# Kernel tuning notes

Hardware: AMD Instinct MI355X
Metric: run time of the kernel (lower is better)

The kernel has to match this reference:

```python
import jax, jax.numpy as jnp
import numpy as np


def _gcn_conv(x, W, b, src, dst, n_nodes):
    """PyG-style GCNConv: XW, symmetric deg^-1/2 normalization over edges
    (with self-loops already included in src/dst), scatter-add to targets, + bias."""
    xw = x @ W  # [N, F_out]
    ones = jnp.ones(src.shape[0], dtype=xw.dtype)
    deg = jax.ops.segment_sum(ones, dst, num_segments=n_nodes)  # in-degree incl. self-loops
    dinv = jnp.where(deg > 0, jax.lax.rsqrt(jnp.maximum(deg, 1.0)), 0.0)
    norm = dinv[src] * dinv[dst]                        # [E]
    msgs = xw[src] * norm[:, None]                      # [E, F_out] gather + scale
    out = jax.ops.segment_sum(msgs, dst, num_segments=n_nodes)  # scatter-add
    return out + b


def setup_inputs() -> dict:
    key = jax.random.key(0)
    k1, k2, k3, k4 = jax.random.split(key, 4)
    N, E = 100000, 1600000
    IN, HID, OUT = 128, 64, 64
    x = jax.random.normal(k1, (N, IN), dtype=jnp.float32)
    edge_index = jax.random.randint(k2, (2, E), 0, N, dtype=jnp.int64)
    W1 = jax.random.normal(k3, (IN, HID), dtype=jnp.float32) * (1.0 / np.sqrt(IN))
    b1 = jnp.zeros((HID,), dtype=jnp.float32)
    W2 = jax.random.normal(k4, (HID, OUT), dtype=jnp.float32) * (1.0 / np.sqrt(HID))
    b2 = jnp.zeros((OUT,), dtype=jnp.float32)
    return {"x": x, "edge_index": edge_index, "W1": W1, "b1": b1, "W2": W2, "b2": b2}


def reference(x, edge_index, W1, b1, W2, b2):
    n_nodes = x.shape[0]
    # add self-loops (PyG GCNConv default add_self_loops=True)
    loops = jnp.arange(n_nodes, dtype=edge_index.dtype)
    src = jnp.concatenate([edge_index[0], loops])
    dst = jnp.concatenate([edge_index[1], loops])
    h = _gcn_conv(x, W1, b1, src, dst, n_nodes)
    h = jax.nn.relu(h)
    z = _gcn_conv(h, W2, b2, src, dst, n_nodes)
    return z
```

## Files before the change

kernel.cpp:

```cpp
#include <hip/hip_runtime.h>

#define IN_F 128
#define HID_F 64
#define BKT_SHIFT 9
#define BKT_SIZE 512
#define CHUNK 4096

typedef unsigned short ushort_t;
typedef __attribute__((ext_vector_type(8))) short bf16x8;
typedef __attribute__((ext_vector_type(8))) unsigned short u16x8;
typedef __attribute__((ext_vector_type(4))) float f32x4;

__device__ inline ushort_t f2bf(float f) {
    unsigned u = __float_as_uint(f);
    u += 0x7FFFu + ((u >> 16) & 1u);
    return (ushort_t)(u >> 16);
}
__device__ inline float bf2f(ushort_t u) {
    return __uint_as_float((unsigned)u << 16);
}


__global__ __launch_bounds__(256) void k_hist(const int* __restrict__ dst,
        int* __restrict__ ghist, int E) {
    __shared__ int hist[256];
    int tid = threadIdx.x;
    hist[tid] = 0;
    __syncthreads();
    int e0 = blockIdx.x * CHUNK, e1 = min(e0 + CHUNK, E);
    for (int e = e0 + tid; e < e1; e += 256)
        atomicAdd(&hist[dst[e] >> BKT_SHIFT], 1);
    __syncthreads();
    ghist[blockIdx.x * 256 + tid] = hist[tid];
}

__global__ __launch_bounds__(256) void k_colscan(int* __restrict__ ghist,
        int* __restrict__ gcount, int nb) {
    __shared__ int s[256];
    int t = threadIdx.x;
    int b = blockIdx.x;
    int j0 = 2 * t, j1 = 2 * t + 1;
    int v0 = (j0 < nb) ? ghist[j0 * 256 + b] : 0;
    int v1 = (j1 < nb) ? ghist[j1 * 256 + b] : 0;
    int p = v0 + v1;
    s[t] = p;
    __syncthreads();
    for (int off = 1; off < 256; off <<= 1) {
        int v = (t >= off) ? s[t - off] : 0;
        __syncthreads();
        s[t] += v;
        __syncthreads();
    }
    int excl = s[t] - p;
    if (j0 < nb) ghist[j0 * 256 + b] = excl;
    if (j1 < nb) ghist[j1 * 256 + b] = excl + v0;
    if (t == 255) gcount[b] = s[255];
}

__global__ __launch_bounds__(256) void k_bscan(const int* __restrict__ gcount,
        int* __restrict__ gbase, int* __restrict__ bbase,
        int* __restrict__ rowptr, int N, int E) {
    __shared__ int s[256];
    int t = threadIdx.x;
    int c = gcount[t];
    s[t] = c;
    __syncthreads();
    for (int off = 1; off < 256; off <<= 1) {
        int v = (t >= off) ? s[t - off] : 0;
        __syncthreads();
        s[t] += v;
        __syncthreads();
    }
    int base = s[t] - c;
    gbase[t] = base;
    bbase[t] = base;
    if (t == 255) bbase[256] = s[255];
    if (t == 0) rowptr[N] = E;
}

__global__ __launch_bounds__(256) void k_scatter(const int* __restrict__ src,
        const int* __restrict__ dst, const int* __restrict__ ghist,
        const int* __restrict__ gbase, unsigned* __restrict__ gbin, int E) {
    __shared__ int cur[256];
    int tid = threadIdx.x;
    cur[tid] = ghist[blockIdx.x * 256 + tid] + gbase[tid];
    __syncthreads();
    int e0 = blockIdx.x * CHUNK, e1 = min(e0 + CHUNK, E);
    for (int e = e0 + tid; e < e1; e += 256) {
        int d = dst[e];
        int b = d >> BKT_SHIFT;
        int p = atomicAdd(&cur[b], 1);
        gbin[p] = ((unsigned)(d & (BKT_SIZE - 1)) << 23) | (unsigned)src[e];
    }
}

__global__ __launch_bounds__(256) void k_fill2(const unsigned* __restrict__ gbin,
        const int* __restrict__ bbase, int* __restrict__ rowptr,
        float* __restrict__ dinv, int* __restrict__ col, int N) {
    __shared__ int cnt[BKT_SIZE];
    __shared__ int pos[BKT_SIZE];
    __shared__ int s[256];
    int tid = threadIdx.x;
    int b = blockIdx.x;
    int e0 = bbase[b], e1 = bbase[b + 1];
    cnt[tid] = 0; cnt[tid + 256] = 0;
    __syncthreads();
    for (int e = e0 + tid; e < e1; e += 256)
        atomicAdd(&cnt[gbin[e] >> 23], 1);
    __syncthreads();
    int c0 = cnt[2 * tid], c1 = cnt[2 * tid + 1];
    int p2 = c0 + c1;
    s[tid] = p2;
    __syncthreads();
    for (int off = 1; off < 256; off <<= 1) {
        int v = (tid >= off) ? s[tid - off] : 0;
        __syncthreads();
        s[tid] += v;
        __syncthreads();
    }
    int excl = s[tid] - p2;
    pos[2 * tid] = excl;
    pos[2 * tid + 1] = excl + c0;
    __syncthreads();
    int n0 = b << BKT_SHIFT;
    #pragma unroll
    for (int i = tid; i < BKT_SIZE; i += 256) {
        int n = n0 + i;
        if (n < N) {
            rowptr[n] = e0 + pos[i];
            dinv[n] = rsqrtf((float)cnt[i] + 1.0f);
        }
    }
    __syncthreads();
    for (int e = e0 + tid; e < e1; e += 256) {
        unsigned v = gbin[e];
        int p = atomicAdd(&pos[v >> 23], 1);
        col[e0 + p] = (int)(v & 0x7FFFFFu);
    }
}

__global__ void k_pack(const float* __restrict__ W1, const float* __restrict__ W2,
                       ushort_t* __restrict__ Bp1, ushort_t* __restrict__ Bp2) {
    int tid = blockIdx.x * 256 + threadIdx.x;
    int id = (tid < 8192) ? tid : tid - 8192;
    int j = id & 7, lane = (id >> 3) & 63, t = (id >> 9) & 3, s = id >> 11;
    int k = s * 32 + ((lane >> 4) << 3) + j;
    int n = t * 16 + (lane & 15);
    if (tid < 8192)        Bp1[id] = f2bf(W1[k * 64 + n]);
    else if (tid < 12288)  Bp2[id] = f2bf(W2[k * 64 + n]);
}

template<int K, typename AT>
__global__ __launch_bounds__(256) void k_gemm_mfma(const AT* __restrict__ A,
        const ushort_t* __restrict__ Bp, const float* __restrict__ dinv,
        ushort_t* __restrict__ out, int N) {
    int wave = threadIdx.x >> 6, lane = threadIdx.x & 63;
    int m = lane & 15, q = lane >> 4;
    int row0 = blockIdx.x * 64 + wave * 16;
    int arow = row0 + m;
    int arowc = (arow < N) ? arow : (N - 1);
    f32x4 acc[4] = {};
    #pragma unroll
    for (int s = 0; s < K / 32; ++s) {
        bf16x8 af;
        if constexpr (sizeof(AT) == 4) {
            const float* ap = (const float*)A + (size_t)arowc * K + s * 32 + q * 8;
            float4 x0 = *(const float4*)ap;
            float4 x1 = *(const float4*)(ap + 4);
            af[0] = (short)f2bf(x0.x); af[1] = (short)f2bf(x0.y);
            af[2] = (short)f2bf(x0.z); af[3] = (short)f2bf(x0.w);
            af[4] = (short)f2bf(x1.x); af[5] = (short)f2bf(x1.y);
            af[6] = (short)f2bf(x1.z); af[7] = (short)f2bf(x1.w);
        } else {
            af = *(const bf16x8*)((const ushort_t*)A + (size_t)arowc * K + s * 32 + q * 8);
        }
        #pragma unroll
        for (int t = 0; t < 4; ++t) {
            bf16x8 bf = *(const bf16x8*)(Bp + (size_t)((s * 4 + t) * 64 + lane) * 8);
            acc[t] = __builtin_amdgcn_mfma_f32_16x16x32_bf16(af, bf, acc[t], 0, 0, 0);
        }
    }
    int orow0 = row0 + q * 4;
    float4 d4 = *(const float4*)(dinv + orow0);
    #pragma unroll
    for (int r = 0; r < 4; ++r) {
        int row = orow0 + r;
        if (row < N) {
            float dn = (r == 0) ? d4.x : (r == 1) ? d4.y : (r == 2) ? d4.z : d4.w;
            #pragma unroll
            for (int t = 0; t < 4; ++t)
                out[(size_t)row * 64 + t * 16 + m] = f2bf(acc[t][r] * dn);
        }
    }
}

__global__ __launch_bounds__(256) void k_aggregate(const ushort_t* __restrict__ xws,
        const int* __restrict__ rowptr, const int* __restrict__ col,
        const float* __restrict__ dinv, const float* __restrict__ bias,
        float* __restrict__ outf, ushort_t* __restrict__ outb, int N, int relu_bf16) {
    int n = (blockIdx.x * 256 + threadIdx.x) >> 3;
    int i = threadIdx.x & 7;
    if (n >= N) return;
    int beg = rowptr[n], end = rowptr[n + 1];
    float dn = dinv[n];
    const ushort_t* base = xws + i * 8;
    u16x8 sv = *(const u16x8*)(base + (size_t)n * 64);
    float a[8];
    #pragma unroll
    for (int k = 0; k < 8; ++k) a[k] = bf2f(sv[k]);
    int e = beg;
    for (; e + 8 <= end; e += 8) {
        int c[8];
        #pragma unroll
        for (int j = 0; j < 8; ++j) c[j] = col[e + j];
        u16x8 v[8];
        #pragma unroll
        for (int j = 0; j < 8; ++j) v[j] = *(const u16x8*)(base + (size_t)c[j] * 64);
        #pragma unroll
        for (int j = 0; j < 8; ++j)
            #pragma unroll
            for (int k = 0; k < 8; ++k) a[k] += bf2f(v[j][k]);
    }
    if (e + 4 <= end) {
        int c[4];
        #pragma unroll
        for (int j = 0; j < 4; ++j) c[j] = col[e + j];
        u16x8 v[4];
        #pragma unroll
        for (int j = 0; j < 4; ++j) v[j] = *(const u16x8*)(base + (size_t)c[j] * 64);
        #pragma unroll
        for (int j = 0; j < 4; ++j)
            #pragma unroll
            for (int k = 0; k < 8; ++k) a[k] += bf2f(v[j][k]);
        e += 4;
    }
    for (; e < end; ++e) {
        u16x8 v = *(const u16x8*)(base + (size_t)col[e] * 64);
        #pragma unroll
        for (int k = 0; k < 8; ++k) a[k] += bf2f(v[k]);
    }
    float4 b0 = *(const float4*)(bias + i * 8);
    float4 b1 = *(const float4*)(bias + i * 8 + 4);
    float r[8];
    r[0] = dn * a[0] + b0.x; r[1] = dn * a[1] + b0.y;
    r[2] = dn * a[2] + b0.z; r[3] = dn * a[3] + b0.w;
    r[4] = dn * a[4] + b1.x; r[5] = dn * a[5] + b1.y;
    r[6] = dn * a[6] + b1.z; r[7] = dn * a[7] + b1.w;
    if (relu_bf16) {
        u16x8 o;
        #pragma unroll
        for (int k = 0; k < 8; ++k) o[k] = f2bf(fmaxf(r[k], 0.f));
        *(u16x8*)(outb + (size_t)n * 64 + i * 8) = o;
    } else {
        float4 o0 = {r[0], r[1], r[2], r[3]};
        float4 o1 = {r[4], r[5], r[6], r[7]};
        *(float4*)(outf + (size_t)n * 64 + i * 8) = o0;
        *(float4*)(outf + (size_t)n * 64 + i * 8 + 4) = o1;
    }
}


extern "C" void kernel_launch(void* const* d_in, const int* in_sizes, int n_in,
                              void* d_out, int out_size, void* d_ws, size_t ws_size,
                              hipStream_t stream) {
    const float* x  = (const float*)d_in[0];
    const int*   ei = (const int*)d_in[1];
    const float* W1 = (const float*)d_in[2];
    const float* b1 = (const float*)d_in[3];
    const float* W2 = (const float*)d_in[4];
    const float* b2 = (const float*)d_in[5];
    float* out = (float*)d_out;

    const int N = in_sizes[0] / IN_F;
    const int E = in_sizes[1] / 2;
    const int* src = ei;
    const int* dst = ei + E;

    char* ws = (char*)d_ws;
    const size_t MB = 1u << 20;
    int*      bbase   = (int*)     (ws + 4096);
    int*      gbase   = (int*)     (ws + 8192);
    int*      gcount  = (int*)     (ws + 12288);
    ushort_t* Bp1     = (ushort_t*)(ws + 16384);
    ushort_t* Bp2     = (ushort_t*)(ws + 49152);
    int*      rowptr  = (int*)     (ws + 1 * MB);
    float*    dinv    = (float*)   (ws + 2 * MB);
    unsigned* gbin    = (unsigned*)(ws + 3 * MB);
    int*      ghist   = (int*)     (ws + 10 * MB);
    int*      col     = (int*)     (ws + 11 * MB);
    ushort_t* xws     = (ushort_t*)(ws + 20 * MB);
    ushort_t* h       = (ushort_t*)(ws + 36 * MB);

    const int nbE = (E + CHUNK - 1) / CHUNK;
    const int nbB = (N + BKT_SIZE - 1) / BKT_SIZE;
    const int nbG = (N + 63) / 64;
    const int nbA = (N * 8 + 255) / 256;

    k_pack   <<<48, 256, 0, stream>>>(W1, W2, Bp1, Bp2);
    k_hist   <<<nbE, 256, 0, stream>>>(dst, ghist, E);
    k_colscan<<<256, 256, 0, stream>>>(ghist, gcount, nbE);
    k_bscan  <<<1, 256, 0, stream>>>(gcount, gbase, bbase, rowptr, N, E);
    k_scatter<<<nbE, 256, 0, stream>>>(src, dst, ghist, gbase, gbin, E);
    k_fill2  <<<nbB, 256, 0, stream>>>(gbin, bbase, rowptr, dinv, col, N);

    k_gemm_mfma<IN_F, float>   <<<nbG, 256, 0, stream>>>(x, Bp1, dinv, xws, N);
    k_aggregate<<<nbA, 256, 0, stream>>>(xws, rowptr, col, dinv, b1, nullptr, h, N, 1);

    k_gemm_mfma<HID_F, ushort_t><<<nbG, 256, 0, stream>>>(h, Bp2, dinv, xws, N);
    k_aggregate<<<nbA, 256, 0, stream>>>(xws, rowptr, col, dinv, b2, out, nullptr, N, 0);
}
```

Baseline: 235.4 us.

## Fuse pack into histogram, merge bucket scan via last-block, shrink buckets, add nontemporal hints

The weight-packing kernel is folded into the histogram launch as extra blocks. The bucket-base scan becomes a last-block-done tail of the column scan, driven by an atomic counter, which removes two launches. Buckets shrink to 256 nodes (512 buckets), so the per-bucket fill kernel needs only a single 256-wide scan. Nontemporal load and store hints are added across the streaming kernels. The changes cut launch overhead and improve fill occupancy, at the cost of a doubled histogram size and reliance on the cross-block atomic completion pattern.

```diff
diff --git a/kernel.cpp b/kernel.cpp
--- a/kernel.cpp
+++ b/kernel.cpp
@@ -2,8 +2,9 @@
 
 #define IN_F 128
 #define HID_F 64
-#define BKT_SHIFT 9
-#define BKT_SIZE 512
+#define BKT_SHIFT 8
+#define BKT_SIZE 256
+#define NBKT 512
 #define CHUNK 4096
 
 typedef unsigned short ushort_t;
@@ -21,27 +22,44 @@
 }
 
 
-__global__ __launch_bounds__(256) void k_hist(const int* __restrict__ dst,
-        int* __restrict__ ghist, int E) {
-    __shared__ int hist[256];
+__global__ __launch_bounds__(256) void k_hist_pack(const int* __restrict__ dst,
+        int* __restrict__ ghist, int E, int nbE,
+        const float* __restrict__ W1, const float* __restrict__ W2,
+        ushort_t* __restrict__ Bp1, ushort_t* __restrict__ Bp2,
+        int* __restrict__ done) {
     int tid = threadIdx.x;
-    hist[tid] = 0;
+    if ((int)blockIdx.x >= nbE) {
+        int id = ((int)blockIdx.x - nbE) * 256 + tid;
+        if (id == 0) *done = 0;
+        int iw = (id < 8192) ? id : id - 8192;
+        int j = iw & 7, lane = (iw >> 3) & 63, t = (iw >> 9) & 3, s = iw >> 11;
+        int k = s * 32 + ((lane >> 4) << 3) + j;
+        int n = t * 16 + (lane & 15);
+        if (id < 8192)        Bp1[iw] = f2bf(W1[k * 64 + n]);
+        else if (id < 12288)  Bp2[iw] = f2bf(W2[k * 64 + n]);
+        return;
+    }
+    __shared__ int hist[NBKT];
+    hist[tid] = 0; hist[tid + 256] = 0;
     __syncthreads();
     int e0 = blockIdx.x * CHUNK, e1 = min(e0 + CHUNK, E);
     for (int e = e0 + tid; e < e1; e += 256)
-        atomicAdd(&hist[dst[e] >> BKT_SHIFT], 1);
-    __syncthreads();
-    ghist[blockIdx.x * 256 + tid] = hist[tid];
+        atomicAdd(&hist[__builtin_nontemporal_load(dst + e) >> BKT_SHIFT], 1);
+    __syncthreads();
+    ghist[(size_t)blockIdx.x * NBKT + tid] = hist[tid];
+    ghist[(size_t)blockIdx.x * NBKT + tid + 256] = hist[tid + 256];
 }
 
 __global__ __launch_bounds__(256) void k_colscan(int* __restrict__ ghist,
-        int* __restrict__ gcount, int nb) {
+        int* __restrict__ gcount, int* __restrict__ gbase, int* __restrict__ bbase,
+        int* __restrict__ rowptr, int* __restrict__ done, int nb, int N, int E) {
     __shared__ int s[256];
+    __shared__ int sdone;
     int t = threadIdx.x;
     int b = blockIdx.x;
     int j0 = 2 * t, j1 = 2 * t + 1;
-    int v0 = (j0 < nb) ? ghist[j0 * 256 + b] : 0;
-    int v1 = (j1 < nb) ? ghist[j1 * 256 + b] : 0;
+    int v0 = (j0 < nb) ? ghist[(size_t)j0 * NBKT + b] : 0;
+    int v1 = (j1 < nb) ? ghist[(size_t)j1 * NBKT + b] : 0;
     int p = v0 + v1;
     s[t] = p;
     __syncthreads();
@@ -52,18 +70,21 @@
         __syncthreads();
     }
     int excl = s[t] - p;
-    if (j0 < nb) ghist[j0 * 256 + b] = excl;
-    if (j1 < nb) ghist[j1 * 256 + b] = excl + v0;
-    if (t == 255) gcount[b] = s[255];
-}
-
-__global__ __launch_bounds__(256) void k_bscan(const int* __restrict__ gcount,
-        int* __restrict__ gbase, int* __restrict__ bbase,
-        int* __restrict__ rowptr, int N, int E) {
-    __shared__ int s[256];
-    int t = threadIdx.x;
-    int c = gcount[t];
-    s[t] = c;
+    if (j0 < nb) ghist[(size_t)j0 * NBKT + b] = excl;
+    if (j1 < nb) ghist[(size_t)j1 * NBKT + b] = excl + v0;
+    if (t == 255) atomicExch(&gcount[b], s[255]);
+    __syncthreads();
+    if (t == 0) {
+        __threadfence();
+        sdone = atomicAdd(done, 1);
+    }
+    __syncthreads();
+    if (sdone != (int)gridDim.x - 1) return;
+    int c0 = atomicAdd(&gcount[j0], 0);
+    int c1 = atomicAdd(&gcount[j1], 0);
+    int p2 = c0 + c1;
+    __syncthreads();
+    s[t] = p2;
     __syncthreads();
     for (int off = 1; off < 256; off <<= 1) {
         int v = (t >= off) ? s[t - off] : 0;
@@ -71,26 +92,27 @@
         s[t] += v;
         __syncthreads();
     }
-    int base = s[t] - c;
-    gbase[t] = base;
-    bbase[t] = base;
-    if (t == 255) bbase[256] = s[255];
-    if (t == 0) rowptr[N] = E;
+    int base = s[t] - p2;
+    gbase[j0] = base;       bbase[j0] = base;
+    gbase[j1] = base + c0;  bbase[j1] = base + c0;
+    if (t == 255) { bbase[NBKT] = s[255]; rowptr[N] = E; }
 }
 
 __global__ __launch_bounds__(256) void k_scatter(const int* __restrict__ src,
         const int* __restrict__ dst, const int* __restrict__ ghist,
         const int* __restrict__ gbase, unsigned* __restrict__ gbin, int E) {
-    __shared__ int cur[256];
+    __shared__ int cur[NBKT];
     int tid = threadIdx.x;
-    cur[tid] = ghist[blockIdx.x * 256 + tid] + gbase[tid];
+    cur[tid]       = ghist[(size_t)blockIdx.x * NBKT + tid]       + gbase[tid];
+    cur[tid + 256] = ghist[(size_t)blockIdx.x * NBKT + tid + 256] + gbase[tid + 256];
     __syncthreads();
     int e0 = blockIdx.x * CHUNK, e1 = min(e0 + CHUNK, E);
     for (int e = e0 + tid; e < e1; e += 256) {
-        int d = dst[e];
+        int d  = __builtin_nontemporal_load(dst + e);
+        int sc = __builtin_nontemporal_load(src + e);
         int b = d >> BKT_SHIFT;
-        int p = atomicAdd(&cur[b], 1);
-        gbin[p] = ((unsigned)(d & (BKT_SIZE - 1)) << 23) | (unsigned)src[e];
+        int pp = atomicAdd(&cur[b], 1);
+        gbin[pp] = ((unsigned)(d & (BKT_SIZE - 1)) << 23) | (unsigned)sc;
     }
 }
 
@@ -99,55 +121,37 @@
         float* __restrict__ dinv, int* __restrict__ col, int N) {
     __shared__ int cnt[BKT_SIZE];
     __shared__ int pos[BKT_SIZE];
-    __shared__ int s[256];
     int tid = threadIdx.x;
     int b = blockIdx.x;
     int e0 = bbase[b], e1 = bbase[b + 1];
-    cnt[tid] = 0; cnt[tid + 256] = 0;
+    cnt[tid] = 0;
     __syncthreads();
     for (int e = e0 + tid; e < e1; e += 256)
         atomicAdd(&cnt[gbin[e] >> 23], 1);
     __syncthreads();
-    int c0 = cnt[2 * tid], c1 = cnt[2 * tid + 1];
-    int p2 = c0 + c1;
-    s[tid] = p2;
+    int c = cnt[tid];
+    pos[tid] = c;
     __syncthreads();
     for (int off = 1; off < 256; off <<= 1) {
-        int v = (tid >= off) ? s[tid - off] : 0;
-        __syncthreads();
-        s[tid] += v;
-        __syncthreads();
-    }
-    int excl = s[tid] - p2;
-    pos[2 * tid] = excl;
-    pos[2 * tid + 1] = excl + c0;
-    __syncthreads();
-    int n0 = b << BKT_SHIFT;
-    #pragma unroll
-    for (int i = tid; i < BKT_SIZE; i += 256) {
-        int n = n0 + i;
-        if (n < N) {
-            rowptr[n] = e0 + pos[i];
-            dinv[n] = rsqrtf((float)cnt[i] + 1.0f);
-        }
-    }
+        int v = (tid >= off) ? pos[tid - off] : 0;
+        __syncthreads();
+        pos[tid] += v;
+        __syncthreads();
+    }
+    int excl = pos[tid] - c;
+    int n = (b << BKT_SHIFT) + tid;
+    if (n < N) {
+        rowptr[n] = e0 + excl;
+        dinv[n] = rsqrtf((float)c + 1.0f);
+    }
+    __syncthreads();
+    pos[tid] = excl;
     __syncthreads();
     for (int e = e0 + tid; e < e1; e += 256) {
         unsigned v = gbin[e];
         int p = atomicAdd(&pos[v >> 23], 1);
         col[e0 + p] = (int)(v & 0x7FFFFFu);
     }
-}
-
-__global__ void k_pack(const float* __restrict__ W1, const float* __restrict__ W2,
-                       ushort_t* __restrict__ Bp1, ushort_t* __restrict__ Bp2) {
-    int tid = blockIdx.x * 256 + threadIdx.x;
-    int id = (tid < 8192) ? tid : tid - 8192;
-    int j = id & 7, lane = (id >> 3) & 63, t = (id >> 9) & 3, s = id >> 11;
-    int k = s * 32 + ((lane >> 4) << 3) + j;
-    int n = t * 16 + (lane & 15);
-    if (tid < 8192)        Bp1[id] = f2bf(W1[k * 64 + n]);
-    else if (tid < 12288)  Bp2[id] = f2bf(W2[k * 64 + n]);
 }
 
 template<int K, typename AT>
@@ -165,14 +169,15 @@
         bf16x8 af;
         if constexpr (sizeof(AT) == 4) {
             const float* ap = (const float*)A + (size_t)arowc * K + s * 32 + q * 8;
-            float4 x0 = *(const float4*)ap;
-            float4 x1 = *(const float4*)(ap + 4);
-            af[0] = (short)f2bf(x0.x); af[1] = (short)f2bf(x0.y);
-            af[2] = (short)f2bf(x0.z); af[3] = (short)f2bf(x0.w);
-            af[4] = (short)f2bf(x1.x); af[5] = (short)f2bf(x1.y);
-            af[6] = (short)f2bf(x1.z); af[7] = (short)f2bf(x1.w);
+            f32x4 x0 = __builtin_nontemporal_load((const f32x4*)ap);
+            f32x4 x1 = __builtin_nontemporal_load((const f32x4*)(ap + 4));
+            af[0] = (short)f2bf(x0[0]); af[1] = (short)f2bf(x0[1]);
+            af[2] = (short)f2bf(x0[2]); af[3] = (short)f2bf(x0[3]);
+            af[4] = (short)f2bf(x1[0]); af[5] = (short)f2bf(x1[1]);
+            af[6] = (short)f2bf(x1[2]); af[7] = (short)f2bf(x1[3]);
         } else {
-            af = *(const bf16x8*)((const ushort_t*)A + (size_t)arowc * K + s * 32 + q * 8);
+            af = __builtin_nontemporal_load(
+                (const bf16x8*)((const ushort_t*)A + (size_t)arowc * K + s * 32 + q * 8));
         }
         #pragma unroll
         for (int t = 0; t < 4; ++t) {
@@ -189,7 +194,8 @@
             float dn = (r == 0) ? d4.x : (r == 1) ? d4.y : (r == 2) ? d4.z : d4.w;
             #pragma unroll
             for (int t = 0; t < 4; ++t)
-                out[(size_t)row * 64 + t * 16 + m] = f2bf(acc[t][r] * dn);
+                __builtin_nontemporal_store(f2bf(acc[t][r] * dn),
+                                            out + (size_t)row * 64 + t * 16 + m);
         }
     }
 }
@@ -212,7 +218,7 @@
     for (; e + 8 <= end; e += 8) {
         int c[8];
         #pragma unroll
-        for (int j = 0; j < 8; ++j) c[j] = col[e + j];
+        for (int j = 0; j < 8; ++j) c[j] = __builtin_nontemporal_load(col + e + j);
         u16x8 v[8];
         #pragma unroll
         for (int j = 0; j < 8; ++j) v[j] = *(const u16x8*)(base + (size_t)c[j] * 64);
@@ -224,7 +230,7 @@
     if (e + 4 <= end) {
         int c[4];
         #pragma unroll
-        for (int j = 0; j < 4; ++j) c[j] = col[e + j];
+        for (int j = 0; j < 4; ++j) c[j] = __builtin_nontemporal_load(col + e + j);
         u16x8 v[4];
         #pragma unroll
         for (int j = 0; j < 4; ++j) v[j] = *(const u16x8*)(base + (size_t)c[j] * 64);
@@ -250,12 +256,12 @@
         u16x8 o;
         #pragma unroll
         for (int k = 0; k < 8; ++k) o[k] = f2bf(fmaxf(r[k], 0.f));
-        *(u16x8*)(outb + (size_t)n * 64 + i * 8) = o;
+        __builtin_nontemporal_store(o, (u16x8*)(outb + (size_t)n * 64 + i * 8));
     } else {
-        float4 o0 = {r[0], r[1], r[2], r[3]};
-        float4 o1 = {r[4], r[5], r[6], r[7]};
-        *(float4*)(outf + (size_t)n * 64 + i * 8) = o0;
-        *(float4*)(outf + (size_t)n * 64 + i * 8 + 4) = o1;
+        f32x4 o0 = {r[0], r[1], r[2], r[3]};
+        f32x4 o1 = {r[4], r[5], r[6], r[7]};
+        __builtin_nontemporal_store(o0, (f32x4*)(outf + (size_t)n * 64 + i * 8));
+        __builtin_nontemporal_store(o1, (f32x4*)(outf + (size_t)n * 64 + i * 8 + 4));
     }
 }
 
@@ -278,6 +284,7 @@
 
     char* ws = (char*)d_ws;
     const size_t MB = 1u << 20;
+    int*      done    = (int*)     (ws + 0);
     int*      bbase   = (int*)     (ws + 4096);
     int*      gbase   = (int*)     (ws + 8192);
     int*      gcount  = (int*)     (ws + 12288);
@@ -296,12 +303,10 @@
     const int nbG = (N + 63) / 64;
     const int nbA = (N * 8 + 255) / 256;
 
-    k_pack   <<<48, 256, 0, stream>>>(W1, W2, Bp1, Bp2);
-    k_hist   <<<nbE, 256, 0, stream>>>(dst, ghist, E);
-    k_colscan<<<256, 256, 0, stream>>>(ghist, gcount, nbE);
-    k_bscan  <<<1, 256, 0, stream>>>(gcount, gbase, bbase, rowptr, N, E);
-    k_scatter<<<nbE, 256, 0, stream>>>(src, dst, ghist, gbase, gbin, E);
-    k_fill2  <<<nbB, 256, 0, stream>>>(gbin, bbase, rowptr, dinv, col, N);
+    k_hist_pack<<<nbE + 48, 256, 0, stream>>>(dst, ghist, E, nbE, W1, W2, Bp1, Bp2, done);
+    k_colscan  <<<NBKT, 256, 0, stream>>>(ghist, gcount, gbase, bbase, rowptr, done, nbE, N, E);
+    k_scatter  <<<nbE, 256, 0, stream>>>(src, dst, ghist, gbase, gbin, E);
+    k_fill2    <<<nbB, 256, 0, stream>>>(gbin, bbase, rowptr, dinv, col, N);
 
     k_gemm_mfma<IN_F, float>   <<<nbG, 256, 0, stream>>>(x, Bp1, dinv, xws, N);
     k_aggregate<<<nbA, 256, 0, stream>>>(xws, rowptr, col, dinv, b1, nullptr, h, N, 1);
```

Result: slower. 267.9 us (+13.8%).
